# Kernel tuning notes

Measured on AMD Instinct MI355X. Metric: run time of the kernel, lower is better.

Reference implementation:

```python
import jax, jax.numpy as jnp
import numpy as np

B, S, RNN, ATTH = 256, 196, 1024, 512  # batch, att_size, rnn_size, att_h_size


def setup_inputs() -> dict:
    key = jax.random.key(0)
    k1, k2, k3, k4, k5, k6, k7 = jax.random.split(key, 7)
    h = jax.random.normal(k1, (B, RNN), dtype=jnp.float32)
    att_feats = jax.random.normal(k2, (B, S, RNN), dtype=jnp.float32)
    p_att_feats = jax.random.normal(k3, (B, S, ATTH), dtype=jnp.float32)
    # learned params (torch nn.Linear: y = x @ W.T + b)
    w_h2att = jax.random.normal(k4, (ATTH, RNN), dtype=jnp.float32) / np.sqrt(RNN)
    b_h2att = jax.random.normal(k5, (ATTH,), dtype=jnp.float32) * 0.01
    w_alpha = jax.random.normal(k6, (1, ATTH), dtype=jnp.float32) / np.sqrt(ATTH)
    b_alpha = jax.random.normal(k7, (1,), dtype=jnp.float32) * 0.01
    return {
        "h": h,
        "att_feats": att_feats,
        "p_att_feats": p_att_feats,
        "w_h2att": w_h2att,
        "b_h2att": b_h2att,
        "w_alpha": w_alpha,
        "b_alpha": b_alpha,
    }


def reference(h, att_feats, p_att_feats, w_h2att, b_h2att, w_alpha, b_alpha):
    # att_h = h2att(h): [B, ATTH]
    att_h = h @ w_h2att.T + b_h2att
    # additive combine + tanh: [B, S, ATTH]
    dot = jnp.tanh(p_att_feats + att_h[:, None, :])
    # alpha_net: [B, S]
    scores = jnp.einsum("bsa,a->bs", dot, w_alpha[0]) + b_alpha[0]
    weight = jax.nn.softmax(scores, axis=1)
    # weighted sum of att_feats: [B, RNN]
    att_res = jnp.einsum("bs,bsd->bd", weight, att_feats)
    return att_res
```

## Files before the change

kernel.cpp:

```cpp
#include <hip/hip_runtime.h>
#include <cstddef>

static constexpr int kB    = 256;
static constexpr int kS    = 196;
static constexpr int kRNN  = 1024;
static constexpr int kATTH = 512;

__device__ __forceinline__ float fast_tanh(float x) {
    x = fminf(12.0f, fmaxf(-12.0f, x));
    float e = __expf(2.0f * x);
    return __fdividef(e - 1.0f, e + 1.0f);
}

__device__ __forceinline__ float dot8t(const float4 p0, const float4 p1,
                                       const float4 ah0, const float4 ah1,
                                       const float4 wa0, const float4 wa1) {
    float r;
    r  = fast_tanh(p0.x + ah0.x) * wa0.x;
    r += fast_tanh(p0.y + ah0.y) * wa0.y;
    r += fast_tanh(p0.z + ah0.z) * wa0.z;
    r += fast_tanh(p0.w + ah0.w) * wa0.w;
    r += fast_tanh(p1.x + ah1.x) * wa1.x;
    r += fast_tanh(p1.y + ah1.y) * wa1.y;
    r += fast_tanh(p1.z + ah1.z) * wa1.z;
    r += fast_tanh(p1.w + ah1.w) * wa1.w;
    return r;
}

__global__ __launch_bounds__(1024) void att_one(
    const float* __restrict__ h,
    const float* __restrict__ att_feats,
    const float* __restrict__ p_att,
    const float* __restrict__ w_h2att,
    const float* __restrict__ b_h2att,
    const float* __restrict__ w_alpha,
    const float* __restrict__ b_alpha,
    float* __restrict__ out) {
    const int b = blockIdx.x;
    const int tid = threadIdx.x;
    const int lane = tid & 63;
    const int wave = tid >> 6;

    __shared__ float sAttH[kATTH];
    __shared__ float4 sAcc[16][256];
    __shared__ float sSum[16];

    const int col = lane << 3;
    const float* pbase = &p_att[(size_t)b * kS * kATTH + col];
    const float* abase = &att_feats[(size_t)b * kS * kRNN + (lane << 2)];

    int s = wave;
    float4 p0, p1, v0, v1, v2, v3;
    {
        const float* p = pbase + (size_t)s * kATTH;
        p0 = *(const float4*)p;
        p1 = *(const float4*)(p + 4);
        const float* a = abase + (size_t)s * kRNN;
        v0 = *(const float4*)(a);
        v1 = *(const float4*)(a + 256);
        v2 = *(const float4*)(a + 512);
        v3 = *(const float4*)(a + 768);
    }

    {
        const float* hb = &h[(size_t)b * kRNN];
        const int k0 = lane << 2;
        const float4 h0 = *(const float4*)&hb[k0];
        const float4 h1 = *(const float4*)&hb[k0 + 256];
        const float4 h2 = *(const float4*)&hb[k0 + 512];
        const float4 h3 = *(const float4*)&hb[k0 + 768];
        const int abase0 = wave << 5;
#pragma unroll 2
        for (int r = 0; r < 32; ++r) {
            const int a = abase0 + r;
            const float* wr = &w_h2att[(size_t)a * kRNN + k0];
            const float4 x0 = *(const float4*)(wr);
            const float4 x1 = *(const float4*)(wr + 256);
            const float4 x2 = *(const float4*)(wr + 512);
            const float4 x3 = *(const float4*)(wr + 768);
            float d;
            d  = x0.x * h0.x + x0.y * h0.y + x0.z * h0.z + x0.w * h0.w;
            d += x1.x * h1.x + x1.y * h1.y + x1.z * h1.z + x1.w * h1.w;
            d += x2.x * h2.x + x2.y * h2.y + x2.z * h2.z + x2.w * h2.w;
            d += x3.x * h3.x + x3.y * h3.y + x3.z * h3.z + x3.w * h3.w;
#pragma unroll
            for (int off = 32; off > 0; off >>= 1) d += __shfl_xor(d, off, 64);
            if (lane == 0) sAttH[a] = d + b_h2att[a];
        }
    }
    __syncthreads();

    const float4 ah0 = *(const float4*)&sAttH[col];
    const float4 ah1 = *(const float4*)&sAttH[col + 4];
    const float4 wa0 = *(const float4*)&w_alpha[col];
    const float4 wa1 = *(const float4*)&w_alpha[col + 4];
    const float balpha = b_alpha[0];

    float sw = fabsf(wa0.x) + fabsf(wa0.y) + fabsf(wa0.z) + fabsf(wa0.w) +
               fabsf(wa1.x) + fabsf(wa1.y) + fabsf(wa1.z) + fabsf(wa1.w);
#pragma unroll
    for (int off = 32; off > 0; off >>= 1) sw += __shfl_xor(sw, off, 64);
    const float ebias = balpha - (sw + fabsf(balpha));

    float4 acc0 = {0.f, 0.f, 0.f, 0.f}, acc1 = {0.f, 0.f, 0.f, 0.f};
    float4 acc2 = {0.f, 0.f, 0.f, 0.f}, acc3 = {0.f, 0.f, 0.f, 0.f};
    float ssum = 0.f;
    while (true) {
        const int sn = s + 16;
        const bool more = sn < kS;
        float4 np0, np1, nv0, nv1, nv2, nv3;
        if (more) {
            const float* p = pbase + (size_t)sn * kATTH;
            np0 = *(const float4*)p;
            np1 = *(const float4*)(p + 4);
            const float* a = abase + (size_t)sn * kRNN;
            nv0 = *(const float4*)(a);
            nv1 = *(const float4*)(a + 256);
            nv2 = *(const float4*)(a + 512);
            nv3 = *(const float4*)(a + 768);
        }
        float r = dot8t(p0, p1, ah0, ah1, wa0, wa1);
#pragma unroll
        for (int off = 32; off > 0; off >>= 1) r += __shfl_xor(r, off, 64);
        const float e = __expf(r + ebias);
        acc0.x += e * v0.x; acc0.y += e * v0.y; acc0.z += e * v0.z; acc0.w += e * v0.w;
        acc1.x += e * v1.x; acc1.y += e * v1.y; acc1.z += e * v1.z; acc1.w += e * v1.w;
        acc2.x += e * v2.x; acc2.y += e * v2.y; acc2.z += e * v2.z; acc2.w += e * v2.w;
        acc3.x += e * v3.x; acc3.y += e * v3.y; acc3.z += e * v3.z; acc3.w += e * v3.w;
        ssum += e;
        if (!more) break;
        s = sn;
        p0 = np0; p1 = np1;
        v0 = nv0; v1 = nv1; v2 = nv2; v3 = nv3;
    }

    sAcc[wave][(0 << 6) + lane] = acc0;
    sAcc[wave][(1 << 6) + lane] = acc1;
    sAcc[wave][(2 << 6) + lane] = acc2;
    sAcc[wave][(3 << 6) + lane] = acc3;
    if (lane == 0) sSum[wave] = ssum;
    __syncthreads();

    float tot = 0.f;
#pragma unroll
    for (int w = 0; w < 16; ++w) tot += sSum[w];
    const float inv = __fdividef(1.0f, tot);

    const float* sA = (const float*)sAcc;
    float o = 0.f;
#pragma unroll
    for (int w = 0; w < 16; ++w) o += sA[w * 1024 + tid];
    out[(size_t)b * kRNN + tid] = o * inv;
}

extern "C" void kernel_launch(void* const* d_in, const int* in_sizes, int n_in,
                              void* d_out, int out_size, void* d_ws, size_t ws_size,
                              hipStream_t stream) {
    const float* h         = (const float*)d_in[0];
    const float* att_feats = (const float*)d_in[1];
    const float* p_att     = (const float*)d_in[2];
    const float* w_h2att   = (const float*)d_in[3];
    const float* b_h2att   = (const float*)d_in[4];
    const float* w_alpha   = (const float*)d_in[5];
    const float* b_alpha   = (const float*)d_in[6];
    float* out = (float*)d_out;

    att_one<<<kB, 1024, 0, stream>>>(h, att_feats, p_att, w_h2att, b_h2att,
                                     w_alpha, b_alpha, out);
}
```

Before: 389.6 us.

## Split fused attention kernel into four kernels with per-batch sequence splitting

Replaces the single fused per-batch kernel with four launches: the att_h matvec, score computation split four ways over the sequence, a weighted-sum partial pass over att_feats per quarter, and a final combine that normalizes. The aim is more blocks (1024 instead of 256) so more CUs are busy streaming p_att and att_feats. The cost is extra launches, global round trips for att_h, scores and partials, and dropping the overlap between att_feats loads and score compute.

```diff
diff --git a/kernel.cpp b/kernel.cpp
--- a/kernel.cpp
+++ b/kernel.cpp
@@ -5,6 +5,12 @@
 static constexpr int kS    = 196;
 static constexpr int kRNN  = 1024;
 static constexpr int kATTH = 512;
+static constexpr int kQ    = 4;
+static constexpr int kSC   = kS / kQ;
+
+static constexpr size_t kOffAttH  = 0;
+static constexpr size_t kOffEsc   = kOffAttH + (size_t)kB * kATTH;
+static constexpr size_t kOffPart  = kOffEsc + (size_t)kB * kS;
 
 __device__ __forceinline__ float fast_tanh(float x) {
     x = fminf(12.0f, fmaxf(-12.0f, x));
@@ -27,71 +33,53 @@
     return r;
 }
 
-__global__ __launch_bounds__(1024) void att_one(
-    const float* __restrict__ h,
-    const float* __restrict__ att_feats,
-    const float* __restrict__ p_att,
-    const float* __restrict__ w_h2att,
-    const float* __restrict__ b_h2att,
-    const float* __restrict__ w_alpha,
-    const float* __restrict__ b_alpha,
-    float* __restrict__ out) {
+__global__ __launch_bounds__(1024) void k1_atth(
+    const float* __restrict__ h, const float* __restrict__ w_h2att,
+    const float* __restrict__ b_h2att, float* __restrict__ att_h) {
     const int b = blockIdx.x;
     const int tid = threadIdx.x;
     const int lane = tid & 63;
     const int wave = tid >> 6;
 
-    __shared__ float sAttH[kATTH];
-    __shared__ float4 sAcc[16][256];
-    __shared__ float sSum[16];
+    const float* hb = &h[(size_t)b * kRNN];
+    const int k0 = lane << 2;
+    const float4 h0 = *(const float4*)&hb[k0];
+    const float4 h1 = *(const float4*)&hb[k0 + 256];
+    const float4 h2 = *(const float4*)&hb[k0 + 512];
+    const float4 h3 = *(const float4*)&hb[k0 + 768];
+    const int abase = wave << 5;
+#pragma unroll 2
+    for (int r = 0; r < 32; ++r) {
+        const int a = abase + r;
+        const float* wr = &w_h2att[(size_t)a * kRNN + k0];
+        const float4 x0 = *(const float4*)(wr);
+        const float4 x1 = *(const float4*)(wr + 256);
+        const float4 x2 = *(const float4*)(wr + 512);
+        const float4 x3 = *(const float4*)(wr + 768);
+        float d;
+        d  = x0.x * h0.x + x0.y * h0.y + x0.z * h0.z + x0.w * h0.w;
+        d += x1.x * h1.x + x1.y * h1.y + x1.z * h1.z + x1.w * h1.w;
+        d += x2.x * h2.x + x2.y * h2.y + x2.z * h2.z + x2.w * h2.w;
+        d += x3.x * h3.x + x3.y * h3.y + x3.z * h3.z + x3.w * h3.w;
+#pragma unroll
+        for (int off = 32; off > 0; off >>= 1) d += __shfl_xor(d, off, 64);
+        if (lane == 0) att_h[(size_t)b * kATTH + a] = d + b_h2att[a];
+    }
+}
+
+__global__ __launch_bounds__(256) void k2_scores(
+    const float* __restrict__ p_att, const float* __restrict__ att_h,
+    const float* __restrict__ w_alpha, const float* __restrict__ b_alpha,
+    float* __restrict__ escore) {
+    const int b = blockIdx.x >> 2;
+    const int q = blockIdx.x & 3;
+    const int tid = threadIdx.x;
+    const int lane = tid & 63;
+    const int wave = tid >> 6;
 
     const int col = lane << 3;
-    const float* pbase = &p_att[(size_t)b * kS * kATTH + col];
-    const float* abase = &att_feats[(size_t)b * kS * kRNN + (lane << 2)];
-
-    int s = wave;
-    float4 p0, p1, v0, v1, v2, v3;
-    {
-        const float* p = pbase + (size_t)s * kATTH;
-        p0 = *(const float4*)p;
-        p1 = *(const float4*)(p + 4);
-        const float* a = abase + (size_t)s * kRNN;
-        v0 = *(const float4*)(a);
-        v1 = *(const float4*)(a + 256);
-        v2 = *(const float4*)(a + 512);
-        v3 = *(const float4*)(a + 768);
-    }
-
-    {
-        const float* hb = &h[(size_t)b * kRNN];
-        const int k0 = lane << 2;
-        const float4 h0 = *(const float4*)&hb[k0];
-        const float4 h1 = *(const float4*)&hb[k0 + 256];
-        const float4 h2 = *(const float4*)&hb[k0 + 512];
-        const float4 h3 = *(const float4*)&hb[k0 + 768];
-        const int abase0 = wave << 5;
-#pragma unroll 2
-        for (int r = 0; r < 32; ++r) {
-            const int a = abase0 + r;
-            const float* wr = &w_h2att[(size_t)a * kRNN + k0];
-            const float4 x0 = *(const float4*)(wr);
-            const float4 x1 = *(const float4*)(wr + 256);
-            const float4 x2 = *(const float4*)(wr + 512);
-            const float4 x3 = *(const float4*)(wr + 768);
-            float d;
-            d  = x0.x * h0.x + x0.y * h0.y + x0.z * h0.z + x0.w * h0.w;
-            d += x1.x * h1.x + x1.y * h1.y + x1.z * h1.z + x1.w * h1.w;
-            d += x2.x * h2.x + x2.y * h2.y + x2.z * h2.z + x2.w * h2.w;
-            d += x3.x * h3.x + x3.y * h3.y + x3.z * h3.z + x3.w * h3.w;
-#pragma unroll
-            for (int off = 32; off > 0; off >>= 1) d += __shfl_xor(d, off, 64);
-            if (lane == 0) sAttH[a] = d + b_h2att[a];
-        }
-    }
-    __syncthreads();
-
-    const float4 ah0 = *(const float4*)&sAttH[col];
-    const float4 ah1 = *(const float4*)&sAttH[col + 4];
+    const float4 ah0 = *(const float4*)&att_h[(size_t)b * kATTH + col];
+    const float4 ah1 = *(const float4*)&att_h[(size_t)b * kATTH + col + 4];
     const float4 wa0 = *(const float4*)&w_alpha[col];
     const float4 wa1 = *(const float4*)&w_alpha[col + 4];
     const float balpha = b_alpha[0];
@@ -102,55 +90,85 @@
     for (int off = 32; off > 0; off >>= 1) sw += __shfl_xor(sw, off, 64);
     const float ebias = balpha - (sw + fabsf(balpha));
 
-    float4 acc0 = {0.f, 0.f, 0.f, 0.f}, acc1 = {0.f, 0.f, 0.f, 0.f};
-    float4 acc2 = {0.f, 0.f, 0.f, 0.f}, acc3 = {0.f, 0.f, 0.f, 0.f};
-    float ssum = 0.f;
+    const float* pbase = &p_att[(size_t)b * kS * kATTH + col];
+    const int send = q * kSC + kSC;
+    int s = q * kSC + wave;
+    float4 p0, p1;
+    {
+        const float* p = pbase + (size_t)s * kATTH;
+        p0 = *(const float4*)p;
+        p1 = *(const float4*)(p + 4);
+    }
     while (true) {
-        const int sn = s + 16;
-        const bool more = sn < kS;
-        float4 np0, np1, nv0, nv1, nv2, nv3;
+        const int sn = s + 4;
+        const bool more = sn < send;
+        float4 np0, np1;
         if (more) {
             const float* p = pbase + (size_t)sn * kATTH;
             np0 = *(const float4*)p;
             np1 = *(const float4*)(p + 4);
-            const float* a = abase + (size_t)sn * kRNN;
-            nv0 = *(const float4*)(a);
-            nv1 = *(const float4*)(a + 256);
-            nv2 = *(const float4*)(a + 512);
-            nv3 = *(const float4*)(a + 768);
         }
         float r = dot8t(p0, p1, ah0, ah1, wa0, wa1);
 #pragma unroll
         for (int off = 32; off > 0; off >>= 1) r += __shfl_xor(r, off, 64);
-        const float e = __expf(r + ebias);
-        acc0.x += e * v0.x; acc0.y += e * v0.y; acc0.z += e * v0.z; acc0.w += e * v0.w;
-        acc1.x += e * v1.x; acc1.y += e * v1.y; acc1.z += e * v1.z; acc1.w += e * v1.w;
-        acc2.x += e * v2.x; acc2.y += e * v2.y; acc2.z += e * v2.z; acc2.w += e * v2.w;
-        acc3.x += e * v3.x; acc3.y += e * v3.y; acc3.z += e * v3.z; acc3.w += e * v3.w;
-        ssum += e;
+        if (lane == 0) escore[(size_t)b * kS + s] = __expf(r + ebias);
         if (!more) break;
         s = sn;
         p0 = np0; p1 = np1;
-        v0 = nv0; v1 = nv1; v2 = nv2; v3 = nv3;
     }
+}
 
-    sAcc[wave][(0 << 6) + lane] = acc0;
-    sAcc[wave][(1 << 6) + lane] = acc1;
-    sAcc[wave][(2 << 6) + lane] = acc2;
-    sAcc[wave][(3 << 6) + lane] = acc3;
-    if (lane == 0) sSum[wave] = ssum;
+__global__ __launch_bounds__(256) void k3_pv(
+    const float* __restrict__ att_feats, const float* __restrict__ escore,
+    float* __restrict__ part) {
+    const int b = blockIdx.x >> 2;
+    const int q = blockIdx.x & 3;
+    const int tid = threadIdx.x;
+
+    __shared__ float sW[kSC];
+    if (tid < kSC) sW[tid] = escore[(size_t)b * kS + q * kSC + tid];
     __syncthreads();
 
-    float tot = 0.f;
+    const float* af =
+        &att_feats[((size_t)b * kS + q * kSC) * kRNN + (tid << 2)];
+    float4 acc = {0.f, 0.f, 0.f, 0.f};
+#pragma unroll 7
+    for (int i = 0; i < kSC; ++i) {
+        const float w = sW[i];
+        const float4 v = *(const float4*)(af + (size_t)i * kRNN);
+        acc.x += w * v.x; acc.y += w * v.y;
+        acc.z += w * v.z; acc.w += w * v.w;
+    }
+    *(float4*)&part[((size_t)(b * kQ + q)) * kRNN + (tid << 2)] = acc;
+}
+
+__global__ __launch_bounds__(256) void k4_combine(
+    const float* __restrict__ part, const float* __restrict__ escore,
+    float* __restrict__ out) {
+    const int b = blockIdx.x;
+    const int tid = threadIdx.x;
+    const int lane = tid & 63;
+    const int wave = tid >> 6;
+
+    __shared__ float sPart[4];
+    float v = (tid < kS) ? escore[(size_t)b * kS + tid] : 0.f;
 #pragma unroll
-    for (int w = 0; w < 16; ++w) tot += sSum[w];
-    const float inv = __fdividef(1.0f, tot);
+    for (int off = 32; off > 0; off >>= 1) v += __shfl_xor(v, off, 64);
+    if (lane == 0) sPart[wave] = v;
+    __syncthreads();
+    const float inv = __fdividef(1.0f, sPart[0] + sPart[1] + sPart[2] + sPart[3]);
 
-    const float* sA = (const float*)sAcc;
-    float o = 0.f;
-#pragma unroll
-    for (int w = 0; w < 16; ++w) o += sA[w * 1024 + tid];
-    out[(size_t)b * kRNN + tid] = o * inv;
+    const float* pb = &part[(size_t)b * kQ * kRNN + (tid << 2)];
+    const float4 a0 = *(const float4*)(pb);
+    const float4 a1 = *(const float4*)(pb + kRNN);
+    const float4 a2 = *(const float4*)(pb + 2 * kRNN);
+    const float4 a3 = *(const float4*)(pb + 3 * kRNN);
+    float4 o;
+    o.x = (a0.x + a1.x + a2.x + a3.x) * inv;
+    o.y = (a0.y + a1.y + a2.y + a3.y) * inv;
+    o.z = (a0.z + a1.z + a2.z + a3.z) * inv;
+    o.w = (a0.w + a1.w + a2.w + a3.w) * inv;
+    *(float4*)&out[(size_t)b * kRNN + (tid << 2)] = o;
 }
 
 extern "C" void kernel_launch(void* const* d_in, const int* in_sizes, int n_in,
@@ -165,6 +183,13 @@
     const float* b_alpha   = (const float*)d_in[6];
     float* out = (float*)d_out;
 
-    att_one<<<kB, 1024, 0, stream>>>(h, att_feats, p_att, w_h2att, b_h2att,
-                                     w_alpha, b_alpha, out);
+    float* ws     = (float*)d_ws;
+    float* att_h  = ws + kOffAttH;
+    float* escore = ws + kOffEsc;
+    float* part   = ws + kOffPart;
+
+    k1_atth<<<kB, 1024, 0, stream>>>(h, w_h2att, b_h2att, att_h);
+    k2_scores<<<kB * kQ, 256, 0, stream>>>(p_att, att_h, w_alpha, b_alpha, escore);
+    k3_pv<<<kB * kQ, 256, 0, stream>>>(att_feats, escore, part);
+    k4_combine<<<kB, 256, 0, stream>>>(part, escore, out);
 }
```

After: 398.3 us. 1.02x slower.
